# Performance work log

Hardware: AMD Instinct MI355X
Metric: run time of the kernel (lower is better)

## Reference

```python
import jax, jax.numpy as jnp
import numpy as np

N_NODES = 100000
N_EDGES = 1600000
D = 128


def setup_inputs() -> dict:
    key = jax.random.key(0)
    ks = jax.random.split(key, 9)
    inp = {
        "embs": jax.random.normal(ks[0], (N_NODES, D), dtype=jnp.float32),
        "edge_index0": jax.random.randint(ks[1], (2, N_EDGES), 0, N_NODES, dtype=jnp.int64 if jax.config.jax_enable_x64 else jnp.int32),
        "edge_index1": jax.random.randint(ks[2], (2, N_EDGES), 0, N_NODES, dtype=jnp.int64 if jax.config.jax_enable_x64 else jnp.int32),
        "w_l0": jax.random.normal(ks[3], (D, D), dtype=jnp.float32) * (1.0 / np.sqrt(D)),
        "w_r0": jax.random.normal(ks[4], (D, D), dtype=jnp.float32) * (1.0 / np.sqrt(D)),
        "b0": jnp.zeros((D,), dtype=jnp.float32),
        "w_l1": jax.random.normal(ks[5], (D, D), dtype=jnp.float32) * (1.0 / np.sqrt(D)),
        "w_r1": jax.random.normal(ks[6], (D, D), dtype=jnp.float32) * (1.0 / np.sqrt(D)),
        "b1": jnp.zeros((D,), dtype=jnp.float32),
    }
    return inp


def _sage_conv(x, edge_index, w_l, w_r, b):
    # PyG SAGEConv: out[i] = lin_l(mean_{j->i} x[j]) + lin_r(x[i])
    src, dst = edge_index[0], edge_index[1]
    n = x.shape[0]
    msg = jnp.take(x, src, axis=0)                                  # [E, D] gather
    summed = jax.ops.segment_sum(msg, dst, num_segments=n)          # [N, D] scatter-add
    cnt = jax.ops.segment_sum(jnp.ones(src.shape, x.dtype), dst, num_segments=n)
    agg = summed / jnp.maximum(cnt, 1.0)[:, None]                   # mean; 0 for isolated nodes
    return agg @ w_l.T + b + x @ w_r.T


def reference(embs, edge_index0, edge_index1, w_l0, w_r0, b0, w_l1, w_r1, b1):
    # layer 0 (not last): dropout (eval -> identity) + GELU (torch default = exact erf)
    x = _sage_conv(embs, edge_index0, w_l0, w_r0, b0)
    x = jax.nn.gelu(x, approximate=False)
    # layer 1 (last): no dropout / activation
    x = _sage_conv(x, edge_index1, w_l1, w_r1, b1)
    return x
```

## Files before the change

kernel.cpp:

```cpp
#include <hip/hip_runtime.h>
#include <hip/hip_fp16.h>
#include <math.h>

#define D 128
#define SH 9
#define BW (1 << SH)
#define EPT 16

typedef _Float16 half4v __attribute__((ext_vector_type(4)));
typedef _Float16 half8  __attribute__((ext_vector_type(8)));
typedef float    floatx16 __attribute__((ext_vector_type(16)));

typedef __attribute__((address_space(3))) uint32_t lds_u32_t;
typedef const __attribute__((address_space(1))) uint32_t g_u32_t;

__global__ __launch_bounds__(256) void cast_half(
        const float* __restrict__ x, _Float16* __restrict__ y, int n) {
    int i = blockIdx.x * 256 + threadIdx.x;
    int idx = i * 4;
    if (idx >= n) return;
    float4 v = *(const float4*)(x + idx);
    half4v h;
    h[0] = (_Float16)v.x; h[1] = (_Float16)v.y;
    h[2] = (_Float16)v.z; h[3] = (_Float16)v.w;
    *(half4v*)(y + idx) = h;
}

__global__ __launch_bounds__(256) void prep_bswz2(
        const float* __restrict__ wl0, const float* __restrict__ wr0,
        const float* __restrict__ wl1, const float* __restrict__ wr1,
        _Float16* __restrict__ B0, _Float16* __restrict__ B1) {
    int gid = blockIdx.x * 256 + threadIdx.x;
    if (gid >= 2 * 64 * 512) return;
    int layer = gid >> 15;
    int idx = gid & 32767;
    const float* wl = layer ? wl1 : wl0;
    const float* wr = layer ? wr1 : wr0;
    _Float16* B = layer ? B1 : B0;
    int j = idx & 7;
    int lane = (idx >> 3) & 63;
    int f = idx >> 9;
    int ks = f >> 2, cb = f & 3;
    int k = ks * 16 + (lane >> 5) * 8 + j;
    int c = cb * 32 + (lane & 31);
    float v = (k < 128) ? wl[c * 128 + k] : wr[c * 128 + (k - 128)];
    B[idx] = (_Float16)v;
}

__global__ __launch_bounds__(256) void hist_coarse(
        const int* __restrict__ ei0, const int* __restrict__ ei1,
        int E, int NBK, int* __restrict__ ccnt) {
    __shared__ int h[512];
    int NBIN = 2 * NBK;
    int t = threadIdx.x;
    h[t] = 0; h[t + 256] = 0;
    __syncthreads();
    int t0 = blockIdx.x * (256 * EPT) + t;
#pragma unroll
    for (int k = 0; k < EPT; ++k) {
        int idx = t0 + k * 256;
        if (idx < 2 * E) {
            int g = idx >= E;
            int e = idx - g * E;
            int dst = (g ? ei1 : ei0)[E + e];
            atomicAdd(&h[g * NBK + (dst >> SH)], 1);
        }
    }
    __syncthreads();
    for (int b = t; b < NBIN; b += 256)
        if (h[b]) atomicAdd(&ccnt[b * 16], h[b]);
}

__global__ __launch_bounds__(256) void scan_coarse(
        const int* __restrict__ ccnt, int NBK, int E, int N,
        int* __restrict__ gbase, int* __restrict__ gcur,
        int* __restrict__ rp0, int* __restrict__ rp1) {
    __shared__ int part[256];
    int t = threadIdx.x;
    for (int g = 0; g < 2; ++g) {
        int v = (t < NBK) ? ccnt[(g * NBK + t) * 16] : 0;
        part[t] = v;
        __syncthreads();
        for (int off = 1; off < 256; off <<= 1) {
            int u = (t >= off) ? part[t - off] : 0;
            __syncthreads();
            part[t] += u;
            __syncthreads();
        }
        if (t < NBK) {
            int ex = (t == 0) ? 0 : part[t - 1];
            int b = g * NBK + t;
            gbase[b] = ex;
            gcur[b * 16] = ex;
        }
        __syncthreads();
    }
    if (t == 0) { rp0[N] = E; rp1[N] = E; }
}

__global__ __launch_bounds__(256) void bin_pass1(
        const int* __restrict__ ei0, const int* __restrict__ ei1,
        int E, int NBK, int* __restrict__ gcur,
        int* __restrict__ stage0, int* __restrict__ stage1) {
    __shared__ int cnt[512];
    __shared__ int base[512];
    int NBIN = 2 * NBK;
    int t = threadIdx.x;
    cnt[t] = 0; cnt[t + 256] = 0;
    __syncthreads();
    int t0 = blockIdx.x * (256 * EPT) + t;
    int pk[EPT];
    int bn[EPT];
#pragma unroll
    for (int k = 0; k < EPT; ++k) {
        int idx = t0 + k * 256;
        bn[k] = -1;
        if (idx < 2 * E) {
            int g = idx >= E;
            int e = idx - g * E;
            const int* ei = g ? ei1 : ei0;
            int src = ei[e];
            int dst = ei[E + e];
            pk[k] = src | ((dst & (BW - 1)) << 17);
            bn[k] = g * NBK + (dst >> SH);
            atomicAdd(&cnt[bn[k]], 1);
        }
    }
    __syncthreads();
    for (int b = t; b < NBIN; b += 256) {
        int c = cnt[b];
        base[b] = c ? atomicAdd(&gcur[b * 16], c) : 0;
        cnt[b] = 0;
    }
    __syncthreads();
#pragma unroll
    for (int k = 0; k < EPT; ++k) {
        if (bn[k] >= 0) {
            int b = bn[k];
            int r = atomicAdd(&cnt[b], 1);
            int* stage = (b >= NBK) ? stage1 : stage0;
            stage[base[b] + r] = pk[k];
        }
    }
}

__global__ __launch_bounds__(256) void bin_pass2(
        const int* __restrict__ gbase,
        const int* __restrict__ stage0, const int* __restrict__ stage1,
        int* __restrict__ rp0, int* __restrict__ rp1,
        int* __restrict__ es0, int* __restrict__ es1,
        int N, int NBK, int E) {
    __shared__ int cnt[BW];
    __shared__ int part[256];
    int b = blockIdx.x;
    int g = b >= NBK;
    int bk = b - g * NBK;
    const int* stage = g ? stage1 : stage0;
    int* rp = g ? rp1 : rp0;
    int* es = g ? es1 : es0;
    int lo = bk << SH;
    int hi = min(lo + BW, N);
    int nd = hi - lo;
    int beg = gbase[b];
    int end = (bk == NBK - 1) ? E : gbase[b + 1];
    int t = threadIdx.x;
    cnt[t] = 0; cnt[t + 256] = 0;
    __syncthreads();
    for (int i = beg + t; i < end; i += 256)
        atomicAdd(&cnt[(unsigned)stage[i] >> 17], 1);
    __syncthreads();
    int c0 = cnt[t * 2], c1 = cnt[t * 2 + 1];
    part[t] = c0 + c1;
    __syncthreads();
    for (int off = 1; off < 256; off <<= 1) {
        int u = (t >= off) ? part[t - off] : 0;
        __syncthreads();
        part[t] += u;
        __syncthreads();
    }
    int ex = (t == 0) ? 0 : part[t - 1];
    int base0 = beg + ex;
    if (t * 2 < nd)     rp[lo + t * 2]     = base0;
    if (t * 2 + 1 < nd) rp[lo + t * 2 + 1] = base0 + c0;
    __syncthreads();
    cnt[t * 2] = base0;
    cnt[t * 2 + 1] = base0 + c0;
    __syncthreads();
    int i = beg + t;
    for (; i + 768 < end; i += 1024) {
        unsigned p0 = (unsigned)stage[i];
        unsigned p1 = (unsigned)stage[i + 256];
        unsigned p2 = (unsigned)stage[i + 512];
        unsigned p3 = (unsigned)stage[i + 768];
        int q0 = atomicAdd(&cnt[p0 >> 17], 1);
        int q1 = atomicAdd(&cnt[p1 >> 17], 1);
        int q2 = atomicAdd(&cnt[p2 >> 17], 1);
        int q3 = atomicAdd(&cnt[p3 >> 17], 1);
        es[q0] = p0 & 0x1FFFF;
        es[q1] = p1 & 0x1FFFF;
        es[q2] = p2 & 0x1FFFF;
        es[q3] = p3 & 0x1FFFF;
    }
    for (; i < end; i += 256) {
        unsigned p = (unsigned)stage[i];
        int q = atomicAdd(&cnt[p >> 17], 1);
        es[q] = p & 0x1FFFF;
    }
}

__global__ __launch_bounds__(256) void agg_half(
        const _Float16* __restrict__ x, const int* __restrict__ row_ptr,
        const int* __restrict__ edge_src, _Float16* __restrict__ agg, int N) {
    int gt = blockIdx.x * 256 + threadIdx.x;
    int w = gt >> 6;
    int lane = gt & 63;
    if (w >= N) return;
    int beg = row_ptr[w];
    int end = row_ptr[w + 1];
    int grp = lane >> 5;
    int c   = lane & 31;
    unsigned co = (unsigned)c * 8u;
    const char* xb = (const char*)x;
    float ax = 0.f, ay = 0.f, az = 0.f, aw = 0.f;
    float one = 1.0f;

    for (int chunk = beg; chunk < end; chunk += 64) {
        int n = min(64, end - chunk);
        int iv = (lane < n) ? edge_src[chunk + lane] : -1;
        for (int e = 0; e < n; e += 8) {
            int s[4];
            uint2 v[4];
#pragma unroll
            for (int j = 0; j < 4; ++j)
                s[j] = __shfl(iv, e + 2 * j + grp);
#pragma unroll
            for (int j = 0; j < 4; ++j) {
                v[j] = make_uint2(0u, 0u);
                if (s[j] >= 0)
                    v[j] = *(const uint2*)(xb + (unsigned)s[j] * 256u + co);
            }
#pragma unroll
            for (int j = 0; j < 4; ++j) {
                asm("v_fma_mix_f32 %0, %1, %2, %0 op_sel:[0,0,0] op_sel_hi:[1,0,0]"
                    : "+v"(ax) : "v"(v[j].x), "v"(one));
                asm("v_fma_mix_f32 %0, %1, %2, %0 op_sel:[1,0,0] op_sel_hi:[1,0,0]"
                    : "+v"(ay) : "v"(v[j].x), "v"(one));
                asm("v_fma_mix_f32 %0, %1, %2, %0 op_sel:[0,0,0] op_sel_hi:[1,0,0]"
                    : "+v"(az) : "v"(v[j].y), "v"(one));
                asm("v_fma_mix_f32 %0, %1, %2, %0 op_sel:[1,0,0] op_sel_hi:[1,0,0]"
                    : "+v"(aw) : "v"(v[j].y), "v"(one));
            }
        }
    }

    ax += __shfl_xor(ax, 32);
    ay += __shfl_xor(ay, 32);
    az += __shfl_xor(az, 32);
    aw += __shfl_xor(aw, 32);

    int deg = end - beg;
    float inv = (deg > 0) ? 1.0f / (float)deg : 0.0f;
    if (lane < 32) {
        half4v h;
        h[0] = (_Float16)(ax * inv);
        h[1] = (_Float16)(ay * inv);
        h[2] = (_Float16)(az * inv);
        h[3] = (_Float16)(aw * inv);
        *(half4v*)((char*)agg + (size_t)w * 256 + co) = h;
    }
}

__device__ __forceinline__ float gelu_fast(float v) {
    float z = v * 0.70710678118654752f;
    float s = fabsf(z);
    float t = __builtin_amdgcn_rcpf(fmaf(0.3275911f, s, 1.0f));
    float poly = t * fmaf(t, fmaf(t, fmaf(t, fmaf(t, 1.061405429f,
                      -1.453152027f), 1.421413741f), -0.284496736f),
                      0.254829592f);
    float e = __builtin_amdgcn_exp2f(-1.4426950408889634f * s * s);
    float erfv = copysignf(fmaf(-poly, e, 1.0f), z);
    return 0.5f * v * (1.0f + erfv);
}

template <bool GELU, typename OutT>
__global__ __launch_bounds__(256, 3) void sage_mfma(
        const _Float16* __restrict__ aggh, const _Float16* __restrict__ xh,
        const _Float16* __restrict__ Bswz, const float* __restrict__ bias,
        OutT* __restrict__ out, int N) {
    __shared__ uint4 a_lds[32 * 65];

    const int tid = threadIdx.x;
    const int n0 = blockIdx.x * 64;
    const int wave = tid >> 6;
    const int lane = tid & 63;
    const int l31 = lane & 31;
    const int lhi = lane >> 5;
    const int wr = wave >> 1;
    const int wc = wave & 1;

    if (n0 + 64 <= N) {
#pragma unroll
        for (int i = 0; i < 8; ++i) {
            int c = wave * 8 + i;
            const _Float16* srcb = (c < 16) ? aggh : xh;
            int r0 = n0 + 4 * (c & 15);
            const char* g = (const char*)srcb + (size_t)r0 * 256 + lane * 16;
            uint32_t* l = (uint32_t*)((char*)a_lds + c * 1040);
            __builtin_amdgcn_global_load_lds((g_u32_t*)g, (lds_u32_t*)l,
                                             16, 0, 0);
        }
    } else {
#pragma unroll
        for (int i = 0; i < 8; ++i) {
            int c = wave * 8 + i;
            const _Float16* srcb = (c < 16) ? aggh : xh;
            int grow = n0 + 4 * (c & 15) + (lane >> 4);
            uint4 v = make_uint4(0u, 0u, 0u, 0u);
            if (grow < N)
                v = *(const uint4*)((const char*)srcb + (size_t)grow * 256
                                    + (lane & 15) * 16);
            *(uint4*)((char*)a_lds + c * 1040 + lane * 16) = v;
        }
    }

    half8 breg[2][8][2];
#pragma unroll
    for (int ph = 0; ph < 2; ++ph)
#pragma unroll
        for (int ks = 0; ks < 8; ++ks)
#pragma unroll
            for (int c2 = 0; c2 < 2; ++c2)
                breg[ph][ks][c2] = *(const half8*)(
                    Bswz + (size_t)ph * 16384
                         + ((ks * 4) + (wc * 2 + c2)) * 512 + lane * 8);
#pragma unroll
    for (int ph = 0; ph < 2; ++ph)
#pragma unroll
        for (int ks = 0; ks < 8; ++ks)
#pragma unroll
            for (int c2 = 0; c2 < 2; ++c2)
                asm volatile("" : "+v"(breg[ph][ks][c2]));

    floatx16 acc[2];
#pragma unroll
    for (int c2 = 0; c2 < 2; ++c2)
#pragma unroll
        for (int r = 0; r < 16; ++r) acc[c2][r] = 0.0f;

    __syncthreads();

#pragma unroll
    for (int ph = 0; ph < 2; ++ph)
#pragma unroll
        for (int ks = 0; ks < 8; ++ks) {
            int r = ph * 64 + wr * 32 + l31;
            int abyte = (r >> 2) * 1040 + (r & 3) * 256
                        + ks * 32 + lhi * 16;
            half8 af = *(const half8*)((const char*)a_lds + abyte);
            acc[0] = __builtin_amdgcn_mfma_f32_32x32x16_f16(
                af, breg[ph][ks][0], acc[0], 0, 0, 0);
            acc[1] = __builtin_amdgcn_mfma_f32_32x32x16_f16(
                af, breg[ph][ks][1], acc[1], 0, 0, 0);
        }

#pragma unroll
    for (int c2 = 0; c2 < 2; ++c2) {
        int col = (wc * 2 + c2) * 32 + l31;
        float bv = bias[col];
#pragma unroll
        for (int r = 0; r < 16; ++r) {
            int rowin = (r & 3) + 8 * (r >> 2) + 4 * lhi;
            int grow = n0 + wr * 32 + rowin;
            if (grow < N) {
                float v = acc[c2][r] + bv;
                if (GELU) v = gelu_fast(v);
                out[(size_t)grow * 128 + col] = (OutT)v;
            }
        }
    }
}

extern "C" void kernel_launch(void* const* d_in, const int* in_sizes, int n_in,
                              void* d_out, int out_size, void* d_ws, size_t ws_size,
                              hipStream_t stream) {
    const float* embs = (const float*)d_in[0];
    const int*   ei0  = (const int*)d_in[1];
    const int*   ei1  = (const int*)d_in[2];
    const float* w_l0 = (const float*)d_in[3];
    const float* w_r0 = (const float*)d_in[4];
    const float* b0   = (const float*)d_in[5];
    const float* w_l1 = (const float*)d_in[6];
    const float* w_r1 = (const float*)d_in[7];
    const float* b1   = (const float*)d_in[8];
    float* out = (float*)d_out;

    const int N = in_sizes[0] / D;
    const int E = in_sizes[1] / 2;
    const int NBK = (N + BW - 1) >> SH;
    const int NBIN = 2 * NBK;

    _Float16* x_h   = (_Float16*)d_ws;
    _Float16* h_h   = x_h + (size_t)N * D;
    _Float16* agg_h = h_h + (size_t)N * D;
    _Float16* Bswz0 = agg_h + (size_t)N * D;
    _Float16* Bswz1 = Bswz0 + 64 * 512;
    int* rp0   = (int*)(Bswz1 + 64 * 512);
    int* rp1   = rp0 + (N + 1);
    int* es0   = rp1 + (N + 1);
    int* es1   = es0 + E;
    int* ccnt  = es1 + E;
    int* gbase = ccnt + NBIN * 16;
    int* gcur  = gbase + NBIN;
    int* stage0 = (int*)agg_h;
    int* stage1 = stage0 + E;

    const int cast_grid = ((size_t)N * D / 4 + 255) / 256;
    const int bin_grid  = (2 * E + 256 * EPT - 1) / (256 * EPT);
    const int agg_grid  = ((size_t)N * 64 + 255) / 256;
    const int gemm_grid = (N + 63) / 64;

    cast_half<<<cast_grid, 256, 0, stream>>>(embs, x_h, N * D);
    prep_bswz2<<<256, 256, 0, stream>>>(w_l0, w_r0, w_l1, w_r1, Bswz0, Bswz1);

    hipMemsetAsync(ccnt, 0, (size_t)NBIN * 16 * sizeof(int), stream);
    hist_coarse<<<bin_grid, 256, 0, stream>>>(ei0, ei1, E, NBK, ccnt);
    scan_coarse<<<1, 256, 0, stream>>>(ccnt, NBK, E, N, gbase, gcur, rp0, rp1);
    bin_pass1<<<bin_grid, 256, 0, stream>>>(ei0, ei1, E, NBK, gcur,
                                            stage0, stage1);
    bin_pass2<<<NBIN, 256, 0, stream>>>(gbase, stage0, stage1,
                                        rp0, rp1, es0, es1, N, NBK, E);

    agg_half<<<agg_grid, 256, 0, stream>>>(x_h, rp0, es0, agg_h, N);
    sage_mfma<true, _Float16><<<gemm_grid, 256, 0, stream>>>(
        agg_h, x_h, Bswz0, b0, h_h, N);

    agg_half<<<agg_grid, 256, 0, stream>>>(h_h, rp1, es1, agg_h, N);
    sage_mfma<false, float><<<gemm_grid, 256, 0, stream>>>(
        agg_h, h_h, Bswz1, b1, out, N);
}
```

Baseline: 388.7 us.

## Fuse neighbor mean aggregation into the MFMA SAGE kernel via LDS

Removes the separate aggregation kernel and computes each node's neighbor mean inside the GEMM block, writing it straight into the LDS A-tile instead of round-tripping through a global fp16 agg buffer. Each wave now aggregates 16 rows sequentially, then computes one 32-column slice of the output for all 64 rows, so the wave-to-tile mapping changes. This saves global traffic and two launches. In exchange, gather parallelism per block drops to 4 waves over 64 nodes, and gather latency now overlaps less with the MFMA work.

```diff
diff --git a/kernel.cpp b/kernel.cpp
--- a/kernel.cpp
+++ b/kernel.cpp
@@ -208,68 +208,6 @@
     }
 }
 
-__global__ __launch_bounds__(256) void agg_half(
-        const _Float16* __restrict__ x, const int* __restrict__ row_ptr,
-        const int* __restrict__ edge_src, _Float16* __restrict__ agg, int N) {
-    int gt = blockIdx.x * 256 + threadIdx.x;
-    int w = gt >> 6;
-    int lane = gt & 63;
-    if (w >= N) return;
-    int beg = row_ptr[w];
-    int end = row_ptr[w + 1];
-    int grp = lane >> 5;
-    int c   = lane & 31;
-    unsigned co = (unsigned)c * 8u;
-    const char* xb = (const char*)x;
-    float ax = 0.f, ay = 0.f, az = 0.f, aw = 0.f;
-    float one = 1.0f;
-
-    for (int chunk = beg; chunk < end; chunk += 64) {
-        int n = min(64, end - chunk);
-        int iv = (lane < n) ? edge_src[chunk + lane] : -1;
-        for (int e = 0; e < n; e += 8) {
-            int s[4];
-            uint2 v[4];
-#pragma unroll
-            for (int j = 0; j < 4; ++j)
-                s[j] = __shfl(iv, e + 2 * j + grp);
-#pragma unroll
-            for (int j = 0; j < 4; ++j) {
-                v[j] = make_uint2(0u, 0u);
-                if (s[j] >= 0)
-                    v[j] = *(const uint2*)(xb + (unsigned)s[j] * 256u + co);
-            }
-#pragma unroll
-            for (int j = 0; j < 4; ++j) {
-                asm("v_fma_mix_f32 %0, %1, %2, %0 op_sel:[0,0,0] op_sel_hi:[1,0,0]"
-                    : "+v"(ax) : "v"(v[j].x), "v"(one));
-                asm("v_fma_mix_f32 %0, %1, %2, %0 op_sel:[1,0,0] op_sel_hi:[1,0,0]"
-                    : "+v"(ay) : "v"(v[j].x), "v"(one));
-                asm("v_fma_mix_f32 %0, %1, %2, %0 op_sel:[0,0,0] op_sel_hi:[1,0,0]"
-                    : "+v"(az) : "v"(v[j].y), "v"(one));
-                asm("v_fma_mix_f32 %0, %1, %2, %0 op_sel:[1,0,0] op_sel_hi:[1,0,0]"
-                    : "+v"(aw) : "v"(v[j].y), "v"(one));
-            }
-        }
-    }
-
-    ax += __shfl_xor(ax, 32);
-    ay += __shfl_xor(ay, 32);
-    az += __shfl_xor(az, 32);
-    aw += __shfl_xor(aw, 32);
-
-    int deg = end - beg;
-    float inv = (deg > 0) ? 1.0f / (float)deg : 0.0f;
-    if (lane < 32) {
-        half4v h;
-        h[0] = (_Float16)(ax * inv);
-        h[1] = (_Float16)(ay * inv);
-        h[2] = (_Float16)(az * inv);
-        h[3] = (_Float16)(aw * inv);
-        *(half4v*)((char*)agg + (size_t)w * 256 + co) = h;
-    }
-}
-
 __device__ __forceinline__ float gelu_fast(float v) {
     float z = v * 0.70710678118654752f;
     float s = fabsf(z);
@@ -283,10 +221,10 @@
 }
 
 template <bool GELU, typename OutT>
-__global__ __launch_bounds__(256, 3) void sage_mfma(
-        const _Float16* __restrict__ aggh, const _Float16* __restrict__ xh,
-        const _Float16* __restrict__ Bswz, const float* __restrict__ bias,
-        OutT* __restrict__ out, int N) {
+__global__ __launch_bounds__(256, 3) void fused_sage(
+        const _Float16* __restrict__ xsrc, const int* __restrict__ rp,
+        const int* __restrict__ es, const _Float16* __restrict__ Bswz,
+        const float* __restrict__ bias, OutT* __restrict__ out, int N) {
     __shared__ uint4 a_lds[32 * 65];
 
     const int tid = threadIdx.x;
@@ -295,88 +233,140 @@
     const int lane = tid & 63;
     const int l31 = lane & 31;
     const int lhi = lane >> 5;
-    const int wr = wave >> 1;
-    const int wc = wave & 1;
 
     if (n0 + 64 <= N) {
 #pragma unroll
-        for (int i = 0; i < 8; ++i) {
-            int c = wave * 8 + i;
-            const _Float16* srcb = (c < 16) ? aggh : xh;
+        for (int i = 0; i < 4; ++i) {
+            int c = 16 + wave * 4 + i;
             int r0 = n0 + 4 * (c & 15);
-            const char* g = (const char*)srcb + (size_t)r0 * 256 + lane * 16;
+            const char* g = (const char*)xsrc + (size_t)r0 * 256 + lane * 16;
             uint32_t* l = (uint32_t*)((char*)a_lds + c * 1040);
             __builtin_amdgcn_global_load_lds((g_u32_t*)g, (lds_u32_t*)l,
                                              16, 0, 0);
         }
     } else {
 #pragma unroll
-        for (int i = 0; i < 8; ++i) {
-            int c = wave * 8 + i;
-            const _Float16* srcb = (c < 16) ? aggh : xh;
+        for (int i = 0; i < 4; ++i) {
+            int c = 16 + wave * 4 + i;
             int grow = n0 + 4 * (c & 15) + (lane >> 4);
             uint4 v = make_uint4(0u, 0u, 0u, 0u);
             if (grow < N)
-                v = *(const uint4*)((const char*)srcb + (size_t)grow * 256
+                v = *(const uint4*)((const char*)xsrc + (size_t)grow * 256
                                     + (lane & 15) * 16);
             *(uint4*)((char*)a_lds + c * 1040 + lane * 16) = v;
         }
     }
 
-    half8 breg[2][8][2];
+    half8 breg[2][8];
 #pragma unroll
     for (int ph = 0; ph < 2; ++ph)
 #pragma unroll
         for (int ks = 0; ks < 8; ++ks)
-#pragma unroll
-            for (int c2 = 0; c2 < 2; ++c2)
-                breg[ph][ks][c2] = *(const half8*)(
-                    Bswz + (size_t)ph * 16384
-                         + ((ks * 4) + (wc * 2 + c2)) * 512 + lane * 8);
+            breg[ph][ks] = *(const half8*)(
+                Bswz + (size_t)ph * 16384 + ((ks * 4) + wave) * 512 + lane * 8);
 #pragma unroll
     for (int ph = 0; ph < 2; ++ph)
 #pragma unroll
         for (int ks = 0; ks < 8; ++ks)
-#pragma unroll
-            for (int c2 = 0; c2 < 2; ++c2)
-                asm volatile("" : "+v"(breg[ph][ks][c2]));
+            asm volatile("" : "+v"(breg[ph][ks]));
+
+    {
+        int nb = n0 + wave * 16;
+        int rpi = min(nb + lane, N);
+        int rpv = (lane < 17) ? rp[rpi] : 0;
+        const char* xb = (const char*)xsrc;
+        int grp = lane >> 5;
+        unsigned co = (unsigned)l31 * 8u;
+        float one = 1.0f;
+        for (int k = 0; k < 16; ++k) {
+            int beg = __shfl(rpv, k);
+            int end = __shfl(rpv, k + 1);
+            float ax = 0.f, ay = 0.f, az = 0.f, aw = 0.f;
+            for (int chunk = beg; chunk < end; chunk += 64) {
+                int n = min(64, end - chunk);
+                int iv = (lane < n) ? es[chunk + lane] : -1;
+                for (int e = 0; e < n; e += 8) {
+                    int s[4];
+                    uint2 v[4];
+#pragma unroll
+                    for (int j = 0; j < 4; ++j)
+                        s[j] = __shfl(iv, e + 2 * j + grp);
+#pragma unroll
+                    for (int j = 0; j < 4; ++j) {
+                        v[j] = make_uint2(0u, 0u);
+                        if (s[j] >= 0)
+                            v[j] = *(const uint2*)(xb + (unsigned)s[j] * 256u
+                                                   + co);
+                    }
+#pragma unroll
+                    for (int j = 0; j < 4; ++j) {
+                        asm("v_fma_mix_f32 %0, %1, %2, %0 op_sel:[0,0,0] op_sel_hi:[1,0,0]"
+                            : "+v"(ax) : "v"(v[j].x), "v"(one));
+                        asm("v_fma_mix_f32 %0, %1, %2, %0 op_sel:[1,0,0] op_sel_hi:[1,0,0]"
+                            : "+v"(ay) : "v"(v[j].x), "v"(one));
+                        asm("v_fma_mix_f32 %0, %1, %2, %0 op_sel:[0,0,0] op_sel_hi:[1,0,0]"
+                            : "+v"(az) : "v"(v[j].y), "v"(one));
+                        asm("v_fma_mix_f32 %0, %1, %2, %0 op_sel:[1,0,0] op_sel_hi:[1,0,0]"
+                            : "+v"(aw) : "v"(v[j].y), "v"(one));
+                    }
+                }
+            }
+            ax += __shfl_xor(ax, 32);
+            ay += __shfl_xor(ay, 32);
+            az += __shfl_xor(az, 32);
+            aw += __shfl_xor(aw, 32);
+            int deg = end - beg;
+            float inv = (deg > 0) ? 1.0f / (float)deg : 0.0f;
+            if (lane < 32) {
+                half4v h;
+                h[0] = (_Float16)(ax * inv);
+                h[1] = (_Float16)(ay * inv);
+                h[2] = (_Float16)(az * inv);
+                h[3] = (_Float16)(aw * inv);
+                int r = wave * 16 + k;
+                *(half4v*)((char*)a_lds + (r >> 2) * 1040 + (r & 3) * 256
+                           + co) = h;
+            }
+        }
+    }
 
     floatx16 acc[2];
 #pragma unroll
-    for (int c2 = 0; c2 < 2; ++c2)
-#pragma unroll
-        for (int r = 0; r < 16; ++r) acc[c2][r] = 0.0f;
+    for (int r2 = 0; r2 < 2; ++r2)
+#pragma unroll
+        for (int r = 0; r < 16; ++r) acc[r2][r] = 0.0f;
 
     __syncthreads();
 
 #pragma unroll
     for (int ph = 0; ph < 2; ++ph)
 #pragma unroll
-        for (int ks = 0; ks < 8; ++ks) {
-            int r = ph * 64 + wr * 32 + l31;
-            int abyte = (r >> 2) * 1040 + (r & 3) * 256
-                        + ks * 32 + lhi * 16;
-            half8 af = *(const half8*)((const char*)a_lds + abyte);
-            acc[0] = __builtin_amdgcn_mfma_f32_32x32x16_f16(
-                af, breg[ph][ks][0], acc[0], 0, 0, 0);
-            acc[1] = __builtin_amdgcn_mfma_f32_32x32x16_f16(
-                af, breg[ph][ks][1], acc[1], 0, 0, 0);
-        }
-
-#pragma unroll
-    for (int c2 = 0; c2 < 2; ++c2) {
-        int col = (wc * 2 + c2) * 32 + l31;
+        for (int ks = 0; ks < 8; ++ks)
+#pragma unroll
+            for (int r2 = 0; r2 < 2; ++r2) {
+                int r = ph * 64 + r2 * 32 + l31;
+                int abyte = (r >> 2) * 1040 + (r & 3) * 256
+                            + ks * 32 + lhi * 16;
+                half8 af = *(const half8*)((const char*)a_lds + abyte);
+                acc[r2] = __builtin_amdgcn_mfma_f32_32x32x16_f16(
+                    af, breg[ph][ks], acc[r2], 0, 0, 0);
+            }
+
+    {
+        int col = wave * 32 + l31;
         float bv = bias[col];
 #pragma unroll
-        for (int r = 0; r < 16; ++r) {
-            int rowin = (r & 3) + 8 * (r >> 2) + 4 * lhi;
-            int grow = n0 + wr * 32 + rowin;
-            if (grow < N) {
-                float v = acc[c2][r] + bv;
-                if (GELU) v = gelu_fast(v);
-                out[(size_t)grow * 128 + col] = (OutT)v;
+        for (int r2 = 0; r2 < 2; ++r2)
+#pragma unroll
+            for (int r = 0; r < 16; ++r) {
+                int rowin = (r & 3) + 8 * (r >> 2) + 4 * lhi;
+                int grow = n0 + r2 * 32 + rowin;
+                if (grow < N) {
+                    float v = acc[r2][r] + bv;
+                    if (GELU) v = gelu_fast(v);
+                    out[(size_t)grow * 128 + col] = (OutT)v;
+                }
             }
-        }
     }
 }
 
@@ -416,7 +406,6 @@
 
     const int cast_grid = ((size_t)N * D / 4 + 255) / 256;
     const int bin_grid  = (2 * E + 256 * EPT - 1) / (256 * EPT);
-    const int agg_grid  = ((size_t)N * 64 + 255) / 256;
     const int gemm_grid = (N + 63) / 64;
 
     cast_half<<<cast_grid, 256, 0, stream>>>(embs, x_h, N * D);
@@ -430,11 +419,9 @@
     bin_pass2<<<NBIN, 256, 0, stream>>>(gbase, stage0, stage1,
                                         rp0, rp1, es0, es1, N, NBK, E);
 
-    agg_half<<<agg_grid, 256, 0, stream>>>(x_h, rp0, es0, agg_h, N);
-    sage_mfma<true, _Float16><<<gemm_grid, 256, 0, stream>>>(
-        agg_h, x_h, Bswz0, b0, h_h, N);
-
-    agg_half<<<agg_grid, 256, 0, stream>>>(h_h, rp1, es1, agg_h, N);
-    sage_mfma<false, float><<<gemm_grid, 256, 0, stream>>>(
-        agg_h, h_h, Bswz1, b1, out, N);
-}
+    fused_sage<true, _Float16><<<gemm_grid, 256, 0, stream>>>(
+        x_h, rp0, es0, Bswz0, b0, h_h, N);
+
+    fused_sage<false, float><<<gemm_grid, 256, 0, stream>>>(
+        h_h, rp1, es1, Bswz1, b1, out, N);
+}
```

Result: no change. 391.1 us (+0.6%).
